# Kernel tuning notes

Measured on AMD Instinct MI355X. Metric: run time of the kernel, lower is better.

Reference implementation:

```python
import jax, jax.numpy as jnp
import numpy as np

NUM_CLASSES = 10
EPS = 1e-8  # torch F.cosine_similarity norm clamp


def setup_inputs() -> dict:
    key = jax.random.key(0)
    k1, k2, k3 = jax.random.split(key, 3)
    pred = jax.random.normal(k1, (4096, 128), dtype=jnp.float32)
    target = jax.random.randint(k2, (4096,), 0, NUM_CLASSES, dtype=jnp.int64)
    W = jax.random.normal(k3, (NUM_CLASSES, 128), dtype=jnp.float32)  # cos() class weights
    return {"pred": pred, "target": target, "W": W}


def reference(pred, target, W):
    N, D = pred.shape
    C = NUM_CLASSES
    f32 = pred.dtype

    # pairwise difference norms via GEMM identity (avoids NxNxD tensor)
    sq = jnp.sum(pred * pred, axis=-1)                       # [N]
    G = pred @ pred.T                                        # [N,N]
    d2 = jnp.maximum(sq[:, None] + sq[None, :] - 2.0 * G, 0.0)
    dn = jnp.maximum(jnp.sqrt(d2 + 1e-16), EPS)              # ||f_a - f_b|| clamped

    proj = pred @ W.T                                        # [N,C] = w_i . f
    wn = jnp.maximum(jnp.sqrt(jnp.sum(W * W, axis=-1)), EPS) # [C]

    counts = jnp.zeros((C,), dtype=jnp.int32).at[target].add(1)  # N per class
    exist = jnp.sum(counts > 0).astype(f32)
    Nt = counts[target].astype(f32)                          # N[target[b]] per sample

    loss1 = jnp.zeros((), f32)
    loss2 = jnp.zeros((), f32)
    for i in range(C):
        pos = target == i
        # pair (a in class i, b not in class i); sum order-invariant vs original
        mask = pos[:, None] & (~pos)[None, :]
        Ni = jnp.maximum(counts[i], 1).astype(f32)
        w_pair = jnp.where(mask, 1.0 / (Nt[None, :] * Ni), 0.0)  # 1/(N_j*N_i)
        pi = proj[:, i]
        # cosine_similarity(f_a - f_b, w_i)
        M = (pi[:, None] - pi[None, :]) / (wn[i] * dn)
        l1 = jnp.sum(w_pair * (1.0 - M) ** 2) / (exist - 1.0)
        # detached-margin statistics (same values in forward)
        mm = jnp.sum(w_pair * M) / (exist - 1.0)
        mv = jnp.sum(w_pair * (M - mm) ** 2) / (exist - 1.0)
        valid = counts[i] > 0
        loss1 = loss1 + jnp.where(valid, l1, 0.0)
        loss2 = loss2 + jnp.where(valid, jnp.abs(mv / mm), 0.0)

    loss1 = loss1 / exist
    loss2 = loss2 / exist
    return (loss1, loss2)
```

## Files before the change

### kernel.cpp

```cpp
#include <hip/hip_runtime.h>

#define WS_GCUR   192
#define WS_PART   2048
#define WS_SSQ    65536
#define WS_PROJT  262144
#define WS_SPRED  2097152

#define NCLS 10
#define NROW 4096
#define DDIM 128
#define SLOTS 40960
#define MAXT 42
#define GRID_MAIN (MAXT * MAXT)

typedef __attribute__((ext_vector_type(8))) short short8;
typedef __attribute__((ext_vector_type(4))) float f32x4;

#define AS3(p) ((__attribute__((address_space(3))) void*)(p))
#define AS1(p) ((const __attribute__((address_space(1))) void*)(p))

__device__ __forceinline__ unsigned short f2bf(float x) {
  unsigned int u = __float_as_uint(x);
  u += 0x7FFFu + ((u >> 16) & 1u);
  return (unsigned short)(u >> 16);
}
__device__ __forceinline__ float bf2f(unsigned short b) {
  return __uint_as_float(((unsigned int)b) << 16);
}

__global__ void __launch_bounds__(256)
k_rows(const float* __restrict__ pred, const float* __restrict__ W,
       const int* __restrict__ tgt, char* __restrict__ ws) {
  __shared__ float Wl[NCLS * DDIM];
  __shared__ float invwn_s[NCLS];
  __shared__ int lcnt[NCLS];
  __shared__ int gbase_s[NCLS];
  __shared__ int slot_s[16];
  int t = threadIdx.x;
  if (t < NCLS) lcnt[t] = 0;
  for (int s = t; s < NCLS * DDIM; s += 256) Wl[s] = W[s];
  __syncthreads();

  int myc = 0, lslot = 0;
  if (t < 16) {
    myc = tgt[blockIdx.x * 16 + t];
    lslot = atomicAdd(&lcnt[myc], 1);
  }
  __syncthreads();
  if (t < NCLS) {
    int n = lcnt[t];
    gbase_s[t] = (n > 0) ? atomicAdd((int*)(ws + WS_GCUR + t * 64), n) : 0;
  }
  if (t >= 64 && t < 224) {
    int i = t - 64;
    int c = i >> 4, ln = i & 15;
    float sw = 0.f;
#pragma unroll
    for (int k = 0; k < 8; k++) { float w = Wl[c * DDIM + ln * 8 + k]; sw = fmaf(w, w, sw); }
    sw += __shfl_xor(sw, 1, 64);
    sw += __shfl_xor(sw, 2, 64);
    sw += __shfl_xor(sw, 4, 64);
    sw += __shfl_xor(sw, 8, 64);
    if (ln == 0) invwn_s[c] = 1.0f / fmaxf(sqrtf(sw), 1e-8f);
  }
  __syncthreads();
  if (t < 16) slot_s[t] = myc * (NROW) + gbase_s[myc] + lslot;
  __syncthreads();

  int row  = blockIdx.x * 16 + (t >> 4);
  int part = t & 15;
  int slot = slot_s[t >> 4];
  const float4* p4 = (const float4*)(pred + row * DDIM + part * 8);
  unsigned short* pb = ((unsigned short*)(ws + WS_SPRED)) + slot * DDIM + part * 8;

  float4 v[2];
  float ss = 0.f;
#pragma unroll
  for (int ch = 0; ch < 2; ch++) {
    v[ch] = p4[ch];
    unsigned short b0 = f2bf(v[ch].x), b1 = f2bf(v[ch].y),
                   b2 = f2bf(v[ch].z), b3 = f2bf(v[ch].w);
    float r0 = bf2f(b0), r1 = bf2f(b1), r2 = bf2f(b2), r3 = bf2f(b3);
    ss = fmaf(r0, r0, ss); ss = fmaf(r1, r1, ss);
    ss = fmaf(r2, r2, ss); ss = fmaf(r3, r3, ss);
    ushort4 u; u.x = b0; u.y = b1; u.z = b2; u.w = b3;
    *((ushort4*)(pb + ch * 4)) = u;
  }
  float acc[NCLS];
#pragma unroll
  for (int c = 0; c < NCLS; c++) acc[c] = 0.f;
#pragma unroll
  for (int c = 0; c < NCLS; c++) {
#pragma unroll
    for (int ch = 0; ch < 2; ch++) {
      float4 w = *(const float4*)&Wl[c * DDIM + part * 8 + ch * 4];
      acc[c] = fmaf(v[ch].x, w.x, acc[c]);
      acc[c] = fmaf(v[ch].y, w.y, acc[c]);
      acc[c] = fmaf(v[ch].z, w.z, acc[c]);
      acc[c] = fmaf(v[ch].w, w.w, acc[c]);
    }
  }
#pragma unroll
  for (int m = 1; m <= 8; m <<= 1) {
    ss += __shfl_xor(ss, m, 64);
#pragma unroll
    for (int c = 0; c < NCLS; c++) acc[c] += __shfl_xor(acc[c], m, 64);
  }
  if (part == 0) {
    ((float*)(ws + WS_SSQ))[slot] = ss;
    float* projT = (float*)(ws + WS_PROJT);
#pragma unroll
    for (int c = 0; c < NCLS; c++) projT[c * SLOTS + slot] = acc[c] * invwn_s[c];
  }
}

__global__ void __launch_bounds__(256)
k_main(const char* __restrict__ ws, char* __restrict__ wso) {
  const int t = threadIdx.x;
  int h[NCLS];
#pragma unroll
  for (int c = 0; c < NCLS; c++) h[c] = *((const int*)(ws + WS_GCUR + c * 64));

  int at = blockIdx.x / MAXT, bt = blockIdx.x % MAXT;
  int acc = 0, clsA = 0, ka = 0, clsB = 0, kb = 0;
#pragma unroll
  for (int c = 0; c < NCLS; c++) {
    int tc = (h[c] + 127) >> 7;
    if (at >= acc && at < acc + tc) { clsA = c; ka = at - acc; }
    if (bt >= acc && bt < acc + tc) { clsB = c; kb = bt - acc; }
    acc += tc;
  }
  const int ntiles = acc;
  const bool active = (at < ntiles) && (bt < ntiles) && (clsA != clsB);

  __shared__ __align__(16) char Btile[128 * 256];
  __shared__ float red_s[4][2];
  float p1 = 0.f, p2 = 0.f;

  if (active) {
    const int abase = clsA * NROW + ka * 128;
    const int bbase = clsB * NROW + kb * 128;
    const int avcnt = min(128, h[clsA] - ka * 128);
    const int bvcnt = min(128, h[clsB] - kb * 128);
    const float wg = (1.0f / (float)h[clsA]) * (1.0f / (float)h[clsB]);
    const float INF = __builtin_inff();

    const float* ssq  = (const float*)(ws + WS_SSQ);
    const float* prjA = (const float*)(ws + WS_PROJT) + clsA * SLOTS;
    const unsigned short* spred = (const unsigned short*)(ws + WS_SPRED);

    const int lane = t & 63, w = t >> 6;
    const int l16 = lane & 15, quad = lane >> 4;

#pragma unroll
    for (int it = 0; it < 8; it++) {
      int s = it * 256 + t;
      int r = s >> 4, cg = (s & 15) ^ (r & 15);
      const unsigned short* gp = spred + (bbase + r) * DDIM + cg * 8;
      __builtin_amdgcn_global_load_lds(AS1(gp), AS3(Btile + s * 16), 16, 0, 0);
    }

    float sqbR[8], pnbR[8];
#pragma unroll
    for (int s = 0; s < 8; s++) {
      int bi = s * 16 + l16;
      bool valid = bi < bvcnt;
      sqbR[s] = valid ? ssq[bbase + bi] + 1e-16f : INF;
      pnbR[s] = valid ? prjA[bbase + bi] : 0.0f;
    }

    short8 afrag[2][4];
    f32x4 sqa4[2], pa4[2];
#pragma unroll
    for (int fi = 0; fi < 2; fi++) {
      const unsigned short* ap = spred + (abase + w * 32 + fi * 16 + l16) * DDIM + quad * 8;
#pragma unroll
      for (int kk = 0; kk < 4; kk++) afrag[fi][kk] = *(const short8*)(ap + kk * 32);
      int m0 = w * 32 + fi * 16 + quad * 4;
      sqa4[fi] = *(const f32x4*)(ssq + abase + m0);
      pa4[fi]  = *(const f32x4*)(prjA + abase + m0);
#pragma unroll
      for (int r = 0; r < 4; r++)
        if (m0 + r >= avcnt) sqa4[fi][r] = INF;
    }
    __syncthreads();

    float S1 = 0.f, S2 = 0.f;
#pragma unroll
    for (int s = 0; s < 8; s++) {
      int rb = s * 16 + l16;
      short8 bfrag[4];
#pragma unroll
      for (int kk = 0; kk < 4; kk++)
        bfrag[kk] = *(const short8*)(Btile + rb * 256 + (((quad + kk * 4) ^ l16) * 16));
      float sqb = sqbR[s], pnb = pnbR[s];
#pragma unroll
      for (int fi = 0; fi < 2; fi++) {
        f32x4 g = {0.f, 0.f, 0.f, 0.f};
#pragma unroll
        for (int kk = 0; kk < 4; kk++)
          g = __builtin_amdgcn_mfma_f32_16x16x32_bf16(afrag[fi][kk], bfrag[kk], g, 0, 0, 0);
#pragma unroll
        for (int r = 0; r < 4; r++) {
          float d2 = fmaf(-2.0f, g[r], sqa4[fi][r] + sqb);
          float rin = rsqrtf(d2);
          float M = (pa4[fi][r] - pnb) * rin;
          S1 += M;
          S2 = fmaf(M, M, S2);
        }
      }
    }

#pragma unroll
    for (int off = 32; off > 0; off >>= 1) {
      S1 += __shfl_xor(S1, off, 64);
      S2 += __shfl_xor(S2, off, 64);
    }
    if (lane == 0) { red_s[w][0] = S1; red_s[w][1] = S2; }
    __syncthreads();
    if (t == 0) {
      p1 = wg * ((red_s[0][0] + red_s[1][0]) + (red_s[2][0] + red_s[3][0]));
      p2 = wg * ((red_s[0][1] + red_s[1][1]) + (red_s[2][1] + red_s[3][1]));
    }
  }

  if (t == 0) {
    float* part = (float*)(wso + WS_PART);
    part[blockIdx.x * 2]     = p1;
    part[blockIdx.x * 2 + 1] = p2;
  }
}

__global__ void __launch_bounds__(256)
k_final(const char* __restrict__ ws, float* __restrict__ out) {
  __shared__ float Sred[2 * NCLS];
  __shared__ int tcls_s[MAXT];
  __shared__ int h_s[NCLS];
  int t = threadIdx.x;
  if (t < 2 * NCLS) Sred[t] = 0.f;
  if (t < NCLS) h_s[t] = *((const int*)(ws + WS_GCUR + t * 64));
  __syncthreads();
  if (t == 0) {
    int nb = 0;
    for (int c = 0; c < NCLS; c++) {
      int tc = (h_s[c] + 127) >> 7;
      for (int i = 0; i < tc && nb + i < MAXT; i++) tcls_s[nb + i] = c;
      nb += tc;
    }
    for (int i = nb; i < MAXT; i++) tcls_s[i] = 0;
  }
  __syncthreads();
  const float* part = (const float*)(ws + WS_PART);
  for (int i = t; i < GRID_MAIN; i += 256) {
    int c = tcls_s[i / MAXT];
    float v1 = part[i * 2], v2 = part[i * 2 + 1];
    if (v1 != 0.f || v2 != 0.f) {
      atomicAdd(&Sred[c], v1);
      atomicAdd(&Sred[NCLS + c], v2);
    }
  }
  __syncthreads();
  if (t == 0) {
    float exist = 0.f;
    for (int c = 0; c < NCLS; c++) if (h_s[c] > 0) exist += 1.f;
    float em1 = exist - 1.0f;
    float l1 = 0.f, l2 = 0.f;
    for (int c = 0; c < NCLS; c++) {
      if (h_s[c] <= 0) continue;
      float s1 = Sred[c], s2 = Sred[NCLS + c];
      l1 += (em1 - 2.f * s1 + s2) / em1;
      float mm = s1 / em1;
      float mv = s2 / em1 - mm * mm;
      l2 += fabsf(mv / mm);
    }
    out[0] = l1 / exist;
    out[1] = l2 / exist;
  }
}

extern "C" void kernel_launch(void* const* d_in, const int* in_sizes, int n_in,
                              void* d_out, int out_size, void* d_ws, size_t ws_size,
                              hipStream_t stream) {
  const float* pred = (const float*)d_in[0];
  const int*   tgt  = (const int*)d_in[1];
  const float* W    = (const float*)d_in[2];
  float* out = (float*)d_out;
  char*  ws  = (char*)d_ws;

  hipMemsetAsync(ws, 0, 1024, stream);
  k_rows<<<NROW / 16, 256, 0, stream>>>(pred, W, tgt, ws);
  k_main<<<GRID_MAIN, 256, 0, stream>>>(ws, ws);
  k_final<<<1, 256, 0, stream>>>(ws, out);
}
```

Before: 95.48 us.

## Use deterministic prefix-count slotting, drop memset, load B fragments directly to registers

k_rows now assigns each row its slot by counting earlier targets per class (a prefix scan over tgt) instead of global atomics, and the last block writes the class histogram. This removes the hipMemsetAsync launch and the atomic contention. k_main no longer stages the B tile in LDS through global_load_lds and a barrier. Each lane loads its B fragments straight from global memory into registers, with one-step double buffering. In exchange, later k_rows blocks rescan up to 4096 targets, and B data is no longer shared across the four waves through LDS, so global/L2 traffic rises.

```diff
diff --git a/kernel.cpp b/kernel.cpp
--- a/kernel.cpp
+++ b/kernel.cpp
@@ -1,6 +1,6 @@
 #include <hip/hip_runtime.h>
 
-#define WS_GCUR   192
+#define WS_H      192
 #define WS_PART   2048
 #define WS_SSQ    65536
 #define WS_PROJT  262144
@@ -16,9 +16,6 @@
 typedef __attribute__((ext_vector_type(8))) short short8;
 typedef __attribute__((ext_vector_type(4))) float f32x4;
 
-#define AS3(p) ((__attribute__((address_space(3))) void*)(p))
-#define AS1(p) ((const __attribute__((address_space(1))) void*)(p))
-
 __device__ __forceinline__ unsigned short f2bf(float x) {
   unsigned int u = __float_as_uint(x);
   u += 0x7FFFu + ((u >> 16) & 1u);
@@ -33,30 +30,53 @@
        const int* __restrict__ tgt, char* __restrict__ ws) {
   __shared__ float Wl[NCLS * DDIM];
   __shared__ float invwn_s[NCLS];
-  __shared__ int lcnt[NCLS];
-  __shared__ int gbase_s[NCLS];
+  __shared__ int wred[4][NCLS];
   __shared__ int slot_s[16];
   int t = threadIdx.x;
-  if (t < NCLS) lcnt[t] = 0;
   for (int s = t; s < NCLS * DDIM; s += 256) Wl[s] = W[s];
-  __syncthreads();
-
-  int myc = 0, lslot = 0;
-  if (t < 16) {
-    myc = tgt[blockIdx.x * 16 + t];
-    lslot = atomicAdd(&lcnt[myc], 1);
-  }
-  __syncthreads();
-  if (t < NCLS) {
-    int n = lcnt[t];
-    gbase_s[t] = (n > 0) ? atomicAdd((int*)(ws + WS_GCUR + t * 64), n) : 0;
+
+  const int r0 = blockIdx.x * 16;
+  int cnt[NCLS];
+#pragma unroll
+  for (int c = 0; c < NCLS; c++) cnt[c] = 0;
+  for (int j = t; j < r0; j += 256) {
+    int v = tgt[j];
+#pragma unroll
+    for (int c = 0; c < NCLS; c++) cnt[c] += (v == c) ? 1 : 0;
+  }
+#pragma unroll
+  for (int m = 1; m <= 32; m <<= 1) {
+#pragma unroll
+    for (int c = 0; c < NCLS; c++) cnt[c] += __shfl_xor(cnt[c], m, 64);
+  }
+  const int lane = t & 63, w = t >> 6;
+  if (lane == 0) {
+#pragma unroll
+    for (int c = 0; c < NCLS; c++) wred[w][c] = cnt[c];
+  }
+  __syncthreads();
+
+  if (t == 0) {
+    int base[NCLS];
+#pragma unroll
+    for (int c = 0; c < NCLS; c++)
+      base[c] = wred[0][c] + wred[1][c] + wred[2][c] + wred[3][c];
+    for (int i = 0; i < 16; i++) {
+      int c = tgt[r0 + i];
+      slot_s[i] = c * NROW + base[c];
+      base[c]++;
+    }
+    if (blockIdx.x == gridDim.x - 1) {
+#pragma unroll
+      for (int c = 0; c < NCLS; c++) ((int*)(ws + WS_H))[c] = base[c];
+    }
   }
   if (t >= 64 && t < 224) {
     int i = t - 64;
     int c = i >> 4, ln = i & 15;
     float sw = 0.f;
 #pragma unroll
-    for (int k = 0; k < 8; k++) { float w = Wl[c * DDIM + ln * 8 + k]; sw = fmaf(w, w, sw); }
+    for (int k = 0; k < 8; k++) { float ww = Wl[c * DDIM + ln * 8 + k]; sw = fmaf(ww, ww, sw); }
     sw += __shfl_xor(sw, 1, 64);
     sw += __shfl_xor(sw, 2, 64);
     sw += __shfl_xor(sw, 4, 64);
@@ -64,10 +84,8 @@
     if (ln == 0) invwn_s[c] = 1.0f / fmaxf(sqrtf(sw), 1e-8f);
   }
   __syncthreads();
-  if (t < 16) slot_s[t] = myc * (NROW) + gbase_s[myc] + lslot;
-  __syncthreads();
-
-  int row  = blockIdx.x * 16 + (t >> 4);
+
+  int row  = r0 + (t >> 4);
   int part = t & 15;
   int slot = slot_s[t >> 4];
   const float4* p4 = (const float4*)(pred + row * DDIM + part * 8);
@@ -80,9 +98,9 @@
     v[ch] = p4[ch];
     unsigned short b0 = f2bf(v[ch].x), b1 = f2bf(v[ch].y),
                    b2 = f2bf(v[ch].z), b3 = f2bf(v[ch].w);
-    float r0 = bf2f(b0), r1 = bf2f(b1), r2 = bf2f(b2), r3 = bf2f(b3);
-    ss = fmaf(r0, r0, ss); ss = fmaf(r1, r1, ss);
-    ss = fmaf(r2, r2, ss); ss = fmaf(r3, r3, ss);
+    float r0f = bf2f(b0), r1f = bf2f(b1), r2f = bf2f(b2), r3f = bf2f(b3);
+    ss = fmaf(r0f, r0f, ss); ss = fmaf(r1f, r1f, ss);
+    ss = fmaf(r2f, r2f, ss); ss = fmaf(r3f, r3f, ss);
     ushort4 u; u.x = b0; u.y = b1; u.z = b2; u.w = b3;
     *((ushort4*)(pb + ch * 4)) = u;
   }
@@ -93,11 +111,11 @@
   for (int c = 0; c < NCLS; c++) {
 #pragma unroll
     for (int ch = 0; ch < 2; ch++) {
-      float4 w = *(const float4*)&Wl[c * DDIM + part * 8 + ch * 4];
-      acc[c] = fmaf(v[ch].x, w.x, acc[c]);
-      acc[c] = fmaf(v[ch].y, w.y, acc[c]);
-      acc[c] = fmaf(v[ch].z, w.z, acc[c]);
-      acc[c] = fmaf(v[ch].w, w.w, acc[c]);
+      float4 ww = *(const float4*)&Wl[c * DDIM + part * 8 + ch * 4];
+      acc[c] = fmaf(v[ch].x, ww.x, acc[c]);
+      acc[c] = fmaf(v[ch].y, ww.y, acc[c]);
+      acc[c] = fmaf(v[ch].z, ww.z, acc[c]);
+      acc[c] = fmaf(v[ch].w, ww.w, acc[c]);
     }
   }
 #pragma unroll
@@ -115,11 +133,12 @@
 }
 
 __global__ void __launch_bounds__(256)
-k_main(const char* __restrict__ ws, char* __restrict__ wso) {
+k_main(char* __restrict__ ws) {
   const int t = threadIdx.x;
+  const int* hp = (const int*)(ws + WS_H);
   int h[NCLS];
 #pragma unroll
-  for (int c = 0; c < NCLS; c++) h[c] = *((const int*)(ws + WS_GCUR + c * 64));
+  for (int c = 0; c < NCLS; c++) h[c] = hp[c];
 
   int at = blockIdx.x / MAXT, bt = blockIdx.x % MAXT;
   int acc = 0, clsA = 0, ka = 0, clsB = 0, kb = 0;
@@ -133,7 +152,6 @@
   const int ntiles = acc;
   const bool active = (at < ntiles) && (bt < ntiles) && (clsA != clsB);
 
-  __shared__ __align__(16) char Btile[128 * 256];
   __shared__ float red_s[4][2];
   float p1 = 0.f, p2 = 0.f;
 
@@ -152,14 +170,6 @@
     const int lane = t & 63, w = t >> 6;
     const int l16 = lane & 15, quad = lane >> 4;
 
-#pragma unroll
-    for (int it = 0; it < 8; it++) {
-      int s = it * 256 + t;
-      int r = s >> 4, cg = (s & 15) ^ (r & 15);
-      const unsigned short* gp = spred + (bbase + r) * DDIM + cg * 8;
-      __builtin_amdgcn_global_load_lds(AS1(gp), AS3(Btile + s * 16), 16, 0, 0);
-    }
-
     float sqbR[8], pnbR[8];
 #pragma unroll
     for (int s = 0; s < 8; s++) {
@@ -183,23 +193,27 @@
       for (int r = 0; r < 4; r++)
         if (m0 + r >= avcnt) sqa4[fi][r] = INF;
     }
-    __syncthreads();
+
+    const unsigned short* bb0 = spred + (size_t)(bbase + l16) * DDIM + quad * 8;
+    short8 bcur[4], bnxt[4];
+#pragma unroll
+    for (int kk = 0; kk < 4; kk++) bcur[kk] = *(const short8*)(bb0 + kk * 32);
 
     float S1 = 0.f, S2 = 0.f;
 #pragma unroll
     for (int s = 0; s < 8; s++) {
-      int rb = s * 16 + l16;
-      short8 bfrag[4];
-#pragma unroll
-      for (int kk = 0; kk < 4; kk++)
-        bfrag[kk] = *(const short8*)(Btile + rb * 256 + (((quad + kk * 4) ^ l16) * 16));
+      if (s < 7) {
+        const unsigned short* bp = bb0 + (size_t)(s + 1) * 16 * DDIM;
+#pragma unroll
+        for (int kk = 0; kk < 4; kk++) bnxt[kk] = *(const short8*)(bp + kk * 32);
+      }
       float sqb = sqbR[s], pnb = pnbR[s];
 #pragma unroll
       for (int fi = 0; fi < 2; fi++) {
         f32x4 g = {0.f, 0.f, 0.f, 0.f};
 #pragma unroll
         for (int kk = 0; kk < 4; kk++)
-          g = __builtin_amdgcn_mfma_f32_16x16x32_bf16(afrag[fi][kk], bfrag[kk], g, 0, 0, 0);
+          g = __builtin_amdgcn_mfma_f32_16x16x32_bf16(afrag[fi][kk], bcur[kk], g, 0, 0, 0);
 #pragma unroll
         for (int r = 0; r < 4; r++) {
           float d2 = fmaf(-2.0f, g[r], sqa4[fi][r] + sqb);
@@ -209,6 +223,8 @@
           S2 = fmaf(M, M, S2);
         }
       }
+#pragma unroll
+      for (int kk = 0; kk < 4; kk++) bcur[kk] = bnxt[kk];
     }
 
 #pragma unroll
@@ -225,7 +241,7 @@
   }
 
   if (t == 0) {
-    float* part = (float*)(wso + WS_PART);
+    float* part = (float*)(ws + WS_PART);
     part[blockIdx.x * 2]     = p1;
     part[blockIdx.x * 2 + 1] = p2;
   }
@@ -238,7 +254,7 @@
   __shared__ int h_s[NCLS];
   int t = threadIdx.x;
   if (t < 2 * NCLS) Sred[t] = 0.f;
-  if (t < NCLS) h_s[t] = *((const int*)(ws + WS_GCUR + t * 64));
+  if (t < NCLS) h_s[t] = ((const int*)(ws + WS_H))[t];
   __syncthreads();
   if (t == 0) {
     int nb = 0;
@@ -287,8 +303,7 @@
   float* out = (float*)d_out;
   char*  ws  = (char*)d_ws;
 
-  hipMemsetAsync(ws, 0, 1024, stream);
   k_rows<<<NROW / 16, 256, 0, stream>>>(pred, W, tgt, ws);
-  k_main<<<GRID_MAIN, 256, 0, stream>>>(ws, ws);
+  k_main<<<GRID_MAIN, 256, 0, stream>>>(ws);
   k_final<<<1, 256, 0, stream>>>(ws, out);
 }
```

Result: slower. 116.3 us (+21.8%).

## Enlarge pair tiles to 256x256 with 512-thread blocks and LDS-staged A tile

Applied to the files above, without the earlier changes.

The main pairwise kernel now covers 256x256 sample tiles instead of 128x128, using 512 threads arranged as 4x2 waves. Both the A and B bf16 tiles, plus their squared norms and projections, are staged in LDS through global_load_lds. The goal is fewer blocks, less redundant global traffic for the A operand, and lower per-block overhead. In exchange the kernel uses about 132KB of LDS, which limits occupancy, and padded partial tiles waste more work.

```diff
diff --git a/kernel.cpp b/kernel.cpp
--- a/kernel.cpp
+++ b/kernel.cpp
@@ -1,6 +1,7 @@
 #include <hip/hip_runtime.h>
 
 #define WS_GCUR   192
+#define WS_INVWN  896
 #define WS_PART   2048
 #define WS_SSQ    65536
 #define WS_PROJT  262144
@@ -10,8 +11,9 @@
 #define NROW 4096
 #define DDIM 128
 #define SLOTS 40960
-#define MAXT 42
-#define GRID_MAIN (MAXT * MAXT)
+#define TSZ 256
+#define MAXT2 26
+#define GRID2 (MAXT2 * MAXT2)
 
 typedef __attribute__((ext_vector_type(8))) short short8;
 typedef __attribute__((ext_vector_type(4))) float f32x4;
@@ -64,7 +66,7 @@
     if (ln == 0) invwn_s[c] = 1.0f / fmaxf(sqrtf(sw), 1e-8f);
   }
   __syncthreads();
-  if (t < 16) slot_s[t] = myc * (NROW) + gbase_s[myc] + lslot;
+  if (t < 16) slot_s[t] = myc * NROW + gbase_s[myc] + lslot;
   __syncthreads();
 
   int row  = blockIdx.x * 16 + (t >> 4);
@@ -114,18 +116,18 @@
   }
 }
 
-__global__ void __launch_bounds__(256)
-k_main(const char* __restrict__ ws, char* __restrict__ wso) {
+__global__ void __launch_bounds__(512, 2)
+k_main(char* __restrict__ ws) {
   const int t = threadIdx.x;
   int h[NCLS];
 #pragma unroll
   for (int c = 0; c < NCLS; c++) h[c] = *((const int*)(ws + WS_GCUR + c * 64));
 
-  int at = blockIdx.x / MAXT, bt = blockIdx.x % MAXT;
+  int at = blockIdx.x / MAXT2, bt = blockIdx.x % MAXT2;
   int acc = 0, clsA = 0, ka = 0, clsB = 0, kb = 0;
 #pragma unroll
   for (int c = 0; c < NCLS; c++) {
-    int tc = (h[c] + 127) >> 7;
+    int tc = (h[c] + TSZ - 1) >> 8;
     if (at >= acc && at < acc + tc) { clsA = c; ka = at - acc; }
     if (bt >= acc && bt < acc + tc) { clsB = c; kb = bt - acc; }
     acc += tc;
@@ -133,15 +135,18 @@
   const int ntiles = acc;
   const bool active = (at < ntiles) && (bt < ntiles) && (clsA != clsB);
 
-  __shared__ __align__(16) char Btile[128 * 256];
-  __shared__ float red_s[4][2];
+  __shared__ __align__(16) char Atile[TSZ * 256];
+  __shared__ __align__(16) char Btile[TSZ * 256];
+  __shared__ __align__(16) float sqa_s[TSZ], pa_s[TSZ];
+  __shared__ float sqb_s[TSZ], pnb_s[TSZ];
+  __shared__ float red_s[8][2];
   float p1 = 0.f, p2 = 0.f;
 
   if (active) {
-    const int abase = clsA * NROW + ka * 128;
-    const int bbase = clsB * NROW + kb * 128;
-    const int avcnt = min(128, h[clsA] - ka * 128);
-    const int bvcnt = min(128, h[clsB] - kb * 128);
+    const int abase = clsA * NROW + ka * TSZ;
+    const int bbase = clsB * NROW + kb * TSZ;
+    const int avcnt = min(TSZ, h[clsA] - ka * TSZ);
+    const int bvcnt = min(TSZ, h[clsB] - kb * TSZ);
     const float wg = (1.0f / (float)h[clsA]) * (1.0f / (float)h[clsB]);
     const float INF = __builtin_inff();
 
@@ -149,53 +154,61 @@
     const float* prjA = (const float*)(ws + WS_PROJT) + clsA * SLOTS;
     const unsigned short* spred = (const unsigned short*)(ws + WS_SPRED);
 
+    {
+      int i = t & 255;
+      if (t < 256) {
+        sqa_s[i] = (i < avcnt) ? ssq[abase + i] : INF;
+        pa_s[i]  = prjA[abase + i];
+      } else {
+        sqb_s[i] = (i < bvcnt) ? ssq[bbase + i] + 1e-16f : INF;
+        pnb_s[i] = (i < bvcnt) ? prjA[bbase + i] : 0.0f;
+      }
+    }
+
+#pragma unroll
+    for (int it = 0; it < 8; it++) {
+      int s = it * 512 + t;
+      int r = s >> 4, cg = (s & 15) ^ (r & 15);
+      const unsigned short* gp = spred + (size_t)(abase + r) * DDIM + cg * 8;
+      __builtin_amdgcn_global_load_lds(AS1(gp), AS3(Atile + s * 16), 16, 0, 0);
+    }
+#pragma unroll
+    for (int it = 0; it < 8; it++) {
+      int s = it * 512 + t;
+      int r = s >> 4, cg = (s & 15) ^ (r & 15);
+      const unsigned short* gp = spred + (size_t)(bbase + r) * DDIM + cg * 8;
+      __builtin_amdgcn_global_load_lds(AS1(gp), AS3(Btile + s * 16), 16, 0, 0);
+    }
+    __syncthreads();
+
     const int lane = t & 63, w = t >> 6;
+    const int wr = w >> 1, wc = w & 1;
     const int l16 = lane & 15, quad = lane >> 4;
 
-#pragma unroll
-    for (int it = 0; it < 8; it++) {
-      int s = it * 256 + t;
-      int r = s >> 4, cg = (s & 15) ^ (r & 15);
-      const unsigned short* gp = spred + (bbase + r) * DDIM + cg * 8;
-      __builtin_amdgcn_global_load_lds(AS1(gp), AS3(Btile + s * 16), 16, 0, 0);
-    }
-
-    float sqbR[8], pnbR[8];
+    short8 afrag[4][4];
+    f32x4 sqa4[4], pa4[4];
+#pragma unroll
+    for (int fi = 0; fi < 4; fi++) {
+      int ra = wr * 64 + fi * 16 + l16;
+#pragma unroll
+      for (int kk = 0; kk < 4; kk++)
+        afrag[fi][kk] = *(const short8*)(Atile + ra * 256 + (((quad + 4 * kk) ^ l16) * 16));
+      int m0 = wr * 64 + fi * 16 + quad * 4;
+      sqa4[fi] = *(const f32x4*)(sqa_s + m0);
+      pa4[fi]  = *(const f32x4*)(pa_s + m0);
+    }
+
+    float S1 = 0.f, S2 = 0.f;
 #pragma unroll
     for (int s = 0; s < 8; s++) {
-      int bi = s * 16 + l16;
-      bool valid = bi < bvcnt;
-      sqbR[s] = valid ? ssq[bbase + bi] + 1e-16f : INF;
-      pnbR[s] = valid ? prjA[bbase + bi] : 0.0f;
-    }
-
-    short8 afrag[2][4];
-    f32x4 sqa4[2], pa4[2];
-#pragma unroll
-    for (int fi = 0; fi < 2; fi++) {
-      const unsigned short* ap = spred + (abase + w * 32 + fi * 16 + l16) * DDIM + quad * 8;
-#pragma unroll
-      for (int kk = 0; kk < 4; kk++) afrag[fi][kk] = *(const short8*)(ap + kk * 32);
-      int m0 = w * 32 + fi * 16 + quad * 4;
-      sqa4[fi] = *(const f32x4*)(ssq + abase + m0);
-      pa4[fi]  = *(const f32x4*)(prjA + abase + m0);
-#pragma unroll
-      for (int r = 0; r < 4; r++)
-        if (m0 + r >= avcnt) sqa4[fi][r] = INF;
-    }
-    __syncthreads();
-
-    float S1 = 0.f, S2 = 0.f;
-#pragma unroll
-    for (int s = 0; s < 8; s++) {
-      int rb = s * 16 + l16;
+      int rb = wc * 128 + s * 16 + l16;
       short8 bfrag[4];
 #pragma unroll
       for (int kk = 0; kk < 4; kk++)
-        bfrag[kk] = *(const short8*)(Btile + rb * 256 + (((quad + kk * 4) ^ l16) * 16));
-      float sqb = sqbR[s], pnb = pnbR[s];
-#pragma unroll
-      for (int fi = 0; fi < 2; fi++) {
+        bfrag[kk] = *(const short8*)(Btile + rb * 256 + (((quad + 4 * kk) ^ l16) * 16));
+      float sqb = sqb_s[rb], pnb = pnb_s[rb];
+#pragma unroll
+      for (int fi = 0; fi < 4; fi++) {
         f32x4 g = {0.f, 0.f, 0.f, 0.f};
 #pragma unroll
         for (int kk = 0; kk < 4; kk++)
@@ -219,13 +232,15 @@
     if (lane == 0) { red_s[w][0] = S1; red_s[w][1] = S2; }
     __syncthreads();
     if (t == 0) {
-      p1 = wg * ((red_s[0][0] + red_s[1][0]) + (red_s[2][0] + red_s[3][0]));
-      p2 = wg * ((red_s[0][1] + red_s[1][1]) + (red_s[2][1] + red_s[3][1]));
+      float a1 = 0.f, a2 = 0.f;
+#pragma unroll
+      for (int i = 0; i < 8; i++) { a1 += red_s[i][0]; a2 += red_s[i][1]; }
+      p1 = wg * a1; p2 = wg * a2;
     }
   }
 
   if (t == 0) {
-    float* part = (float*)(wso + WS_PART);
+    float* part = (float*)(ws + WS_PART);
     part[blockIdx.x * 2]     = p1;
     part[blockIdx.x * 2 + 1] = p2;
   }
@@ -234,7 +249,7 @@
 __global__ void __launch_bounds__(256)
 k_final(const char* __restrict__ ws, float* __restrict__ out) {
   __shared__ float Sred[2 * NCLS];
-  __shared__ int tcls_s[MAXT];
+  __shared__ int tcls_s[MAXT2];
   __shared__ int h_s[NCLS];
   int t = threadIdx.x;
   if (t < 2 * NCLS) Sred[t] = 0.f;
@@ -243,16 +258,16 @@
   if (t == 0) {
     int nb = 0;
     for (int c = 0; c < NCLS; c++) {
-      int tc = (h_s[c] + 127) >> 7;
-      for (int i = 0; i < tc && nb + i < MAXT; i++) tcls_s[nb + i] = c;
+      int tc = (h_s[c] + TSZ - 1) >> 8;
+      for (int i = 0; i < tc && nb + i < MAXT2; i++) tcls_s[nb + i] = c;
       nb += tc;
     }
-    for (int i = nb; i < MAXT; i++) tcls_s[i] = 0;
+    for (int i = nb; i < MAXT2; i++) tcls_s[i] = 0;
   }
   __syncthreads();
   const float* part = (const float*)(ws + WS_PART);
-  for (int i = t; i < GRID_MAIN; i += 256) {
-    int c = tcls_s[i / MAXT];
+  for (int i = t; i < GRID2; i += 256) {
+    int c = tcls_s[i / MAXT2];
     float v1 = part[i * 2], v2 = part[i * 2 + 1];
     if (v1 != 0.f || v2 != 0.f) {
       atomicAdd(&Sred[c], v1);
@@ -289,6 +304,6 @@
 
   hipMemsetAsync(ws, 0, 1024, stream);
   k_rows<<<NROW / 16, 256, 0, stream>>>(pred, W, tgt, ws);
-  k_main<<<GRID_MAIN, 256, 0, stream>>>(ws, ws);
+  k_main<<<GRID2, 512, 0, stream>>>(ws);
   k_final<<<1, 256, 0, stream>>>(ws, out);
 }
```

Result: faster. 93.41 us (-2.2%).
